# Optimization experiments

Measured on AMD Instinct MI355X. Metric: run time of the kernel, lower is better.

The kernel has to match this reference:

```python
import jax, jax.numpy as jnp
import numpy as np

B, S, E, H = 2, 4096, 512, 8
D = E // H  # head_dim = 64

def setup_inputs() -> dict:
    key = jax.random.key(0)
    k1, k2 = jax.random.split(key)
    x_local = jax.random.normal(k1, (B, S, E), dtype=jnp.float32)
    # torch nn.Linear weight layout: [out_features, in_features] = [3E, E]
    W_qkv = jax.random.normal(k2, (3 * E, E), dtype=jnp.float32) * (1.0 / np.sqrt(E))
    return {"x_local": x_local, "W_qkv": W_qkv, "segment_len": 2048, "dilation": 1}

def reference(x_local, W_qkv, segment_len, dilation):
    b, s, e = x_local.shape
    h, d = H, D
    # qkv projection (no bias), then split into per-head q,k,v: [b,h,s,d]
    qkv = jnp.einsum('bse,fe->bsf', x_local, W_qkv)
    qkv = qkv.reshape(b, s, 3, h, d).transpose(2, 0, 3, 1, 4)
    q, k, v = qkv[0], qkv[1], qkv[2]
    # dilation==1 -> no slicing branch; world_size==1 -> plain SDPA (no mask)
    scale = 1.0 / np.sqrt(d)
    scores = jnp.einsum('bhqd,bhkd->bhqk', q, k) * scale  # [b,h,s,s]
    attn = jax.nn.softmax(scores, axis=-1)
    out = jnp.einsum('bhqk,bhkd->bhqd', attn, v)
    # [b,h,s,d] -> [b,s,e]
    return out.transpose(0, 2, 1, 3).reshape(b, s, e)
```

## Files before the change

kernel.cpp:

```cpp
#include <hip/hip_runtime.h>
#include <stdint.h>

#define BB 2
#define SS 4096
#define EE 512
#define HH 8
#define DD 64
#define BH 16
#define M_ROWS 8192
#define N_COLS 1536
#define K_DIM 512

typedef unsigned short u16;
typedef unsigned int u32;
typedef __attribute__((ext_vector_type(8))) __bf16 bf16x8;
typedef __attribute__((ext_vector_type(4))) float f32x4;
typedef __attribute__((ext_vector_type(16))) float f32x16;

__device__ __forceinline__ u16 f2bf(float f) {
  u32 u = __float_as_uint(f);
  u32 r = u + 0x7fffu + ((u >> 16) & 1u);
  return (u16)(r >> 16);
}

__device__ __forceinline__ u32 cvtpk(float a, float b) {
  u32 r;
  asm("v_cvt_pk_bf16_f32 %0, %1, %2" : "=v"(r) : "v"(a), "v"(b));
  return r;
}

__device__ __forceinline__ float exp2f_fast(float x) {
  float r;
  asm("v_exp_f32 %0, %1" : "=v"(r) : "v"(x));
  return r;
}

__device__ __forceinline__ void gl_lds16(const void* g, void* l) {
  using gu32 = const __attribute__((address_space(1))) uint32_t;
  using lu32 = __attribute__((address_space(3))) uint32_t;
  __builtin_amdgcn_global_load_lds((gu32*)(uintptr_t)g,
                                   (lu32*)(uint32_t)(uintptr_t)l, 16, 0, 0);
}

__global__ __launch_bounds__(256) void cvt_f32_bf16(const float* __restrict__ src,
                                                    u16* __restrict__ dst, int n) {
  int stride = gridDim.x * blockDim.x * 4;
  for (int i = (blockIdx.x * blockDim.x + threadIdx.x) * 4; i < n; i += stride) {
    float4 v = *(const float4*)(src + i);
    u32 lo = (u32)f2bf(v.x) | ((u32)f2bf(v.y) << 16);
    u32 hi = (u32)f2bf(v.z) | ((u32)f2bf(v.w) << 16);
    uint2 p; p.x = lo; p.y = hi;
    *(uint2*)(dst + i) = p;
  }
}

#define BM 128
#define BN 128
#define BK 64

__global__ __launch_bounds__(256, 3) void qkv_gemm(const u16* __restrict__ Xb,
                                                   const u16* __restrict__ Wb,
                                                   u16* __restrict__ Qg,
                                                   u16* __restrict__ Kg,
                                                   u16* __restrict__ Vt) {
  __shared__ __align__(16) u16 SH[BM * BK * 2];
  u16* Al = SH;
  u16* Bl = SH + BM * BK;

  const int tid = threadIdx.x;
  const int lane = tid & 63;
  const int w = tid >> 6;
  const int wr = w >> 1, wc = w & 1;

  const int flat = blockIdx.x;
  const int sw = (flat & 7) * 96 + (flat >> 3);
  const int bx = sw & 63, by = sw >> 6;
  const int m0 = bx * BM;
  const int n0 = by * BN;

  f32x4 acc[4][4] = {};

  auto STAGE = [&](int kt) {
#pragma unroll
    for (int i = 0; i < 4; i++) {
      int chunk = w * 4 + i;
      int row = chunk * 8 + (lane >> 3);
      int seg = (lane & 7) ^ (row & 7);
      gl_lds16(Xb + (size_t)(m0 + row) * K_DIM + kt * BK + seg * 8, Al + chunk * 512);
      gl_lds16(Wb + (size_t)(n0 + row) * K_DIM + kt * BK + seg * 8, Bl + chunk * 512);
    }
  };

  const int NKT = K_DIM / BK;
  for (int kt = 0; kt < NKT; ++kt) {
    __syncthreads();
    STAGE(kt);
    asm volatile("s_waitcnt vmcnt(0)" ::: "memory");
    __syncthreads();

#pragma unroll
    for (int ks = 0; ks < 2; ++ks) {
      bf16x8 af[4], bfr[4];
#pragma unroll
      for (int t = 0; t < 4; t++) {
        int row = wr * 64 + t * 16 + (lane & 15);
        int byte = row * 128 + (((ks * 64) + (lane >> 4) * 16) ^ ((row & 7) << 4));
        af[t] = *(const bf16x8*)((const char*)Al + byte);
      }
#pragma unroll
      for (int t = 0; t < 4; t++) {
        int row = wc * 64 + t * 16 + (lane & 15);
        int byte = row * 128 + (((ks * 64) + (lane >> 4) * 16) ^ ((row & 7) << 4));
        bfr[t] = *(const bf16x8*)((const char*)Bl + byte);
      }
      __builtin_amdgcn_s_setprio(1);
#pragma unroll
      for (int am = 0; am < 4; am++)
#pragma unroll
        for (int bn = 0; bn < 4; bn++)
          acc[am][bn] = __builtin_amdgcn_mfma_f32_16x16x32_bf16(af[am], bfr[bn], acc[am][bn], 0, 0, 0);
      __builtin_amdgcn_s_setprio(0);
    }
  }

  const float qscale = 0.125f * 1.44269504f;
  if (by < 8) {
#pragma unroll
    for (int am = 0; am < 4; am++) {
      int mbase = m0 + wr * 64 + am * 16 + (lane >> 4) * 4;
#pragma unroll
      for (int bn = 0; bn < 4; bn++) {
        int n = n0 + wc * 64 + bn * 16 + (lane & 15);
        int which = n >> 9;
        int hh = (n >> 6) & 7, dd = n & 63;
        int b = mbase >> 12;
        int bh = b * HH + hh;
        u16* dst = (which == 0) ? Qg : Kg;
        float sc = (which == 0) ? qscale : 1.0f;
#pragma unroll
        for (int i = 0; i < 4; i++) {
          int s = (mbase + i) & 4095;
          dst[((size_t)bh * SS + s) * DD + dd] = f2bf(acc[am][bn][i] * sc);
        }
      }
    }
  } else {
    __syncthreads();
#pragma unroll
    for (int am = 0; am < 4; am++) {
      int mloc = wr * 64 + am * 16 + (lane >> 4) * 4;
#pragma unroll
      for (int bn = 0; bn < 4; bn++) {
        int nl = wc * 64 + bn * 16 + (lane & 15);
        union { u16 h[4]; uint2 u; } pk;
#pragma unroll
        for (int i = 0; i < 4; i++) pk.h[i] = f2bf(acc[am][bn][i]);
        int byte = nl * 256 + ((mloc * 2) ^ ((nl & 7) << 4));
        *(uint2*)((char*)SH + byte) = pk.u;
      }
    }
    __syncthreads();
    const int b = m0 >> 12;
#pragma unroll
    for (int i = 0; i < 8; i++) {
      int c = i * 256 + tid;
      int row = c >> 4, ch = c & 15;
      int byte = row * 256 + ((ch * 16) ^ ((row & 7) << 4));
      uint4 v = *(const uint4*)((const char*)SH + byte);
      int ng = n0 + row;
      int hh = (ng >> 6) & 7, dd = ng & 63;
      *(uint4*)(Vt + ((size_t)(b * HH + hh) * DD + dd) * SS + (m0 & 4095) + ch * 8) = v;
    }
  }
}

#define KVB 64
#define NT (SS / KVB)
#define SPLIT 2
#define HT (NT / SPLIT)

__global__ __launch_bounds__(256, 3) void flash_attn(const u16* __restrict__ Qg,
                                                     const u16* __restrict__ Kg,
                                                     const u16* __restrict__ Vt,
                                                     float* __restrict__ Opart,
                                                     float* __restrict__ Ml) {
  __shared__ __align__(16) char smem[32768];

  const int tid = threadIdx.x;
  const int lane = tid & 63;
  const int w = tid >> 6;
  const int hi = lane >> 5;
  const int lq = lane & 31;
  const int flat = blockIdx.x;
  const int sw = ((flat & 7) << 7) | (flat >> 3);
  const int qx = sw & 31;
  const int bhz = sw >> 5;
  const int bh = bhz >> 1;
  const int z = bhz & 1;
  const int q0 = qx * 128 + w * 32;

  bf16x8 qf[4];
  {
    const u16* qp = Qg + ((size_t)bh * SS + q0 + lq) * DD + hi * 8;
#pragma unroll
    for (int ks = 0; ks < 4; ks++) qf[ks] = *(const bf16x8*)(qp + ks * 16);
  }

  int loff[8];
#pragma unroll
  for (int ks = 0; ks < 4; ks++) {
    int col = ks * 32 + hi * 16;
    loff[ks * 2 + 0] = lq * 128 + (col ^ ((lq & 7) << 4));
    loff[ks * 2 + 1] = (32 + lq) * 128 + (col ^ ((lq & 7) << 4));
  }

  f32x16 oa0 = {}, oa1 = {};
  float m = -1e30f, l = 0.f;

  auto STAGE = [&](int kt, int buf) {
    char* kb = smem + buf * 16384;
    char* vb = kb + 8192;
#pragma unroll
    for (int i = 0; i < 2; i++) {
      int chunk = w * 2 + i;
      int row = chunk * 8 + (lane >> 3);
      int seg = (lane & 7) ^ (row & 7);
      gl_lds16(Kg + ((size_t)bh * SS + (size_t)kt * KVB + row) * DD + seg * 8,
               kb + chunk * 1024);
      gl_lds16(Vt + ((size_t)bh * DD + row) * SS + (size_t)kt * KVB + seg * 8,
               vb + chunk * 1024);
    }
  };

  STAGE(z * HT, 0);
  asm volatile("s_waitcnt vmcnt(0)" ::: "memory");
  __syncthreads();

  for (int t = 0; t < HT; ++t) {
    const int cur = t & 1;
    const char* Kc = smem + cur * 16384;
    const char* Vc = Kc + 8192;

    if (t + 1 < HT) STAGE(z * HT + t + 1, cur ^ 1);

    f32x16 sa0 = {}, sa1 = {};
    __builtin_amdgcn_s_setprio(1);
#pragma unroll
    for (int ks = 0; ks < 4; ks++) {
      bf16x8 kf0 = *(const bf16x8*)(Kc + loff[ks * 2 + 0]);
      bf16x8 kf1 = *(const bf16x8*)(Kc + loff[ks * 2 + 1]);
      sa0 = __builtin_amdgcn_mfma_f32_32x32x16_bf16(kf0, qf[ks], sa0, 0, 0, 0);
      sa1 = __builtin_amdgcn_mfma_f32_32x32x16_bf16(kf1, qf[ks], sa1, 0, 0, 0);
    }
    __builtin_amdgcn_s_setprio(0);

    float c0 = fmaxf(fmaxf(sa0[0], sa0[1]), sa0[2]);
    float c1 = fmaxf(fmaxf(sa0[8], sa0[9]), sa0[10]);
    float c2 = fmaxf(fmaxf(sa1[0], sa1[1]), sa1[2]);
    float c3 = fmaxf(fmaxf(sa1[8], sa1[9]), sa1[10]);
    c0 = fmaxf(fmaxf(c0, sa0[3]), sa0[4]);
    c1 = fmaxf(fmaxf(c1, sa0[11]), sa0[12]);
    c2 = fmaxf(fmaxf(c2, sa1[3]), sa1[4]);
    c3 = fmaxf(fmaxf(c3, sa1[11]), sa1[12]);
    c0 = fmaxf(fmaxf(c0, sa0[5]), sa0[6]);
    c1 = fmaxf(fmaxf(c1, sa0[13]), sa0[14]);
    c2 = fmaxf(fmaxf(c2, sa1[5]), sa1[6]);
    c3 = fmaxf(fmaxf(c3, sa1[13]), sa1[14]);
    c0 = fmaxf(fmaxf(c0, sa0[7]), c2);
    c1 = fmaxf(fmaxf(c1, sa0[15]), c3);
    c0 = fmaxf(fmaxf(c0, sa1[7]), sa1[15]);
    float tm = fmaxf(c0, c1);
    tm = fmaxf(tm, __shfl_xor(tm, 32));
    if (__any(tm > m + 8.f)) {
      float mnew = fmaxf(m, tm);
      float al = exp2f_fast(m - mnew);
      m = mnew;
      l *= al;
      oa0 *= al;
      oa1 *= al;
    }
    sa0 = sa0 - m;
    sa1 = sa1 - m;
#pragma unroll
    for (int r = 0; r < 16; r++) {
      sa0[r] = exp2f_fast(sa0[r]);
      sa1[r] = exp2f_fast(sa1[r]);
    }
    {
      f32x16 ps = sa0 + sa1;
      float rs = (((ps[0] + ps[1]) + (ps[2] + ps[3])) + ((ps[4] + ps[5]) + (ps[6] + ps[7])))
               + (((ps[8] + ps[9]) + (ps[10] + ps[11])) + ((ps[12] + ps[13]) + (ps[14] + ps[15])));
      l += rs;
    }

    bf16x8 paf[4];
#pragma unroll
    for (int kb = 0; kb < 2; kb++) {
#pragma unroll
      for (int h2 = 0; h2 < 2; h2++) {
        int base = h2 * 8;
        u32 a0, b0, a1, b1;
        if (kb == 0) {
          a0 = cvtpk(sa0[base + 0], sa0[base + 1]);
          b0 = cvtpk(sa0[base + 4], sa0[base + 5]);
          a1 = cvtpk(sa0[base + 2], sa0[base + 3]);
          b1 = cvtpk(sa0[base + 6], sa0[base + 7]);
        } else {
          a0 = cvtpk(sa1[base + 0], sa1[base + 1]);
          b0 = cvtpk(sa1[base + 4], sa1[base + 5]);
          a1 = cvtpk(sa1[base + 2], sa1[base + 3]);
          b1 = cvtpk(sa1[base + 6], sa1[base + 7]);
        }
        asm("v_permlane32_swap_b32 %0, %1" : "+v"(a0), "+v"(b0));
        asm("v_permlane32_swap_b32 %0, %1" : "+v"(a1), "+v"(b1));
        union { u32 d[4]; bf16x8 v; } u;
        u.d[0] = a0; u.d[1] = a1; u.d[2] = b0; u.d[3] = b1;
        paf[kb * 2 + h2] = u.v;
      }
    }

    __builtin_amdgcn_s_setprio(1);
#pragma unroll
    for (int ks = 0; ks < 4; ks++) {
      bf16x8 vf0 = *(const bf16x8*)(Vc + loff[ks * 2 + 0]);
      bf16x8 vf1 = *(const bf16x8*)(Vc + loff[ks * 2 + 1]);
      oa0 = __builtin_amdgcn_mfma_f32_32x32x16_bf16(vf0, paf[ks], oa0, 0, 0, 0);
      oa1 = __builtin_amdgcn_mfma_f32_32x32x16_bf16(vf1, paf[ks], oa1, 0, 0, 0);
    }
    __builtin_amdgcn_s_setprio(0);

    asm volatile("s_waitcnt vmcnt(0)" ::: "memory");
    __syncthreads();
  }

  l += __shfl_xor(l, 32);
  if (hi == 0)
    *(float2*)(Ml + ((size_t)(z * BH + bh) * SS + q0 + lq) * 2) = make_float2(m, l);

  float* ow = (float*)(smem + w * 8192);
#pragma unroll
  for (int db = 0; db < 2; db++)
#pragma unroll
    for (int r = 0; r < 16; r++) {
      int d = db * 32 + (r & 3) + 8 * (r >> 2) + 4 * hi;
      float v = db ? oa1[r] : oa0[r];
      *(float*)((char*)ow + lq * 256 + ((d * 4) ^ ((lq & 7) << 4))) = v;
    }
  __syncthreads();
#pragma unroll
  for (int i = 0; i < 8; i++) {
    int c = i * 64 + lane;
    int row = c >> 4, ch = c & 15;
    float4 v = *(const float4*)((const char*)ow + row * 256 + ((ch * 16) ^ ((row & 7) << 4)));
    *(float4*)(Opart + ((size_t)(z * BH + bh) * SS + q0 + row) * DD + ch * 4) = v;
  }
}

__global__ __launch_bounds__(256) void merge_split(const float* __restrict__ Opart,
                                                   const float* __restrict__ Ml,
                                                   float* __restrict__ Out) {
  int idx = blockIdx.x * 256 + threadIdx.x;
  int dq = idx & 15;
  int s = (idx >> 4) & (SS - 1);
  int bh = idx >> 16;
  float2 ml0 = *(const float2*)(Ml + ((size_t)bh * SS + s) * 2);
  float2 ml1 = *(const float2*)(Ml + ((size_t)(BH + bh) * SS + s) * 2);
  float M = fmaxf(ml0.x, ml1.x);
  float e0 = exp2f_fast(ml0.x - M);
  float e1 = exp2f_fast(ml1.x - M);
  float rden = 1.0f / (ml0.y * e0 + ml1.y * e1);
  e0 *= rden; e1 *= rden;
  float4 o0 = *(const float4*)(Opart + ((size_t)bh * SS + s) * DD + dq * 4);
  float4 o1 = *(const float4*)(Opart + ((size_t)(BH + bh) * SS + s) * DD + dq * 4);
  float4 o;
  o.x = o0.x * e0 + o1.x * e1;
  o.y = o0.y * e0 + o1.y * e1;
  o.z = o0.z * e0 + o1.z * e1;
  o.w = o0.w * e0 + o1.w * e1;
  int b = bh >> 3, hh = bh & 7;
  *(float4*)(Out + ((size_t)b * SS + s) * EE + hh * DD + dq * 4) = o;
}

extern "C" void kernel_launch(void* const* d_in, const int* in_sizes, int n_in,
                              void* d_out, int out_size, void* d_ws, size_t ws_size,
                              hipStream_t stream) {
  const float* x = (const float*)d_in[0];
  const float* Wq = (const float*)d_in[1];

  u16* xb = (u16*)d_ws;
  u16* wb = xb + (size_t)M_ROWS * K_DIM;
  u16* Qg = wb + (size_t)N_COLS * K_DIM;
  u16* Kg = Qg + (size_t)BH * SS * DD;
  u16* Vt = Kg + (size_t)BH * SS * DD;
  float* Opart = (float*)(Vt + (size_t)BH * SS * DD);
  float* Ml = Opart + (size_t)SPLIT * BH * SS * DD;

  cvt_f32_bf16<<<2048, 256, 0, stream>>>(x, xb, M_ROWS * K_DIM);
  cvt_f32_bf16<<<768, 256, 0, stream>>>(Wq, wb, N_COLS * K_DIM);

  qkv_gemm<<<768, 256, 0, stream>>>(xb, wb, Qg, Kg, Vt);

  flash_attn<<<1024, 256, 0, stream>>>(Qg, Kg, Vt, Opart, Ml);

  merge_split<<<4096, 256, 0, stream>>>(Opart, Ml, (float*)d_out);
}
```

Before: 190.2 us.

## Split KV into four chunks and store partial outputs in bf16

Raises the flash-attention KV split from two to four, doubling the grid to 2048 blocks, each handling half as many KV tiles. Partial outputs are now written as bf16 instead of fp32 to keep the intermediate traffic from growing. The merge kernel combines four partials with log-sum-exp rescaling. This trades more merge work and bf16 rounding of partials for more parallelism and shorter per-block work on the GPU.

```diff
diff --git a/kernel.cpp b/kernel.cpp
--- a/kernel.cpp
+++ b/kernel.cpp
@@ -35,6 +35,10 @@
   return r;
 }
 
+__device__ __forceinline__ float bf2f(u16 h) {
+  return __uint_as_float((u32)h << 16);
+}
+
 __device__ __forceinline__ void gl_lds16(const void* g, void* l) {
   using gu32 = const __attribute__((address_space(1))) uint32_t;
   using lu32 = __attribute__((address_space(3))) uint32_t;
@@ -176,13 +180,13 @@
 
 #define KVB 64
 #define NT (SS / KVB)
-#define SPLIT 2
+#define SPLIT 4
 #define HT (NT / SPLIT)
 
 __global__ __launch_bounds__(256, 3) void flash_attn(const u16* __restrict__ Qg,
                                                      const u16* __restrict__ Kg,
                                                      const u16* __restrict__ Vt,
-                                                     float* __restrict__ Opart,
+                                                     u16* __restrict__ Opart,
                                                      float* __restrict__ Ml) {
   __shared__ __align__(16) char smem[32768];
 
@@ -192,11 +196,11 @@
   const int hi = lane >> 5;
   const int lq = lane & 31;
   const int flat = blockIdx.x;
-  const int sw = ((flat & 7) << 7) | (flat >> 3);
+  const int sw = ((flat & 7) << 8) | (flat >> 3);
   const int qx = sw & 31;
   const int bhz = sw >> 5;
-  const int bh = bhz >> 1;
-  const int z = bhz & 1;
+  const int bh = bhz >> 2;
+  const int z = bhz & 3;
   const int q0 = qx * 128 + w * 32;
 
   bf16x8 qf[4];
@@ -352,31 +356,44 @@
     int c = i * 64 + lane;
     int row = c >> 4, ch = c & 15;
     float4 v = *(const float4*)((const char*)ow + row * 256 + ((ch * 16) ^ ((row & 7) << 4)));
-    *(float4*)(Opart + ((size_t)(z * BH + bh) * SS + q0 + row) * DD + ch * 4) = v;
-  }
-}
-
-__global__ __launch_bounds__(256) void merge_split(const float* __restrict__ Opart,
+    uint2 p; p.x = cvtpk(v.x, v.y); p.y = cvtpk(v.z, v.w);
+    *(uint2*)(Opart + ((size_t)(z * BH + bh) * SS + q0 + row) * DD + ch * 4) = p;
+  }
+}
+
+__global__ __launch_bounds__(256) void merge_split(const u16* __restrict__ Opart,
                                                    const float* __restrict__ Ml,
                                                    float* __restrict__ Out) {
   int idx = blockIdx.x * 256 + threadIdx.x;
   int dq = idx & 15;
   int s = (idx >> 4) & (SS - 1);
   int bh = idx >> 16;
-  float2 ml0 = *(const float2*)(Ml + ((size_t)bh * SS + s) * 2);
-  float2 ml1 = *(const float2*)(Ml + ((size_t)(BH + bh) * SS + s) * 2);
-  float M = fmaxf(ml0.x, ml1.x);
-  float e0 = exp2f_fast(ml0.x - M);
-  float e1 = exp2f_fast(ml1.x - M);
-  float rden = 1.0f / (ml0.y * e0 + ml1.y * e1);
-  e0 *= rden; e1 *= rden;
-  float4 o0 = *(const float4*)(Opart + ((size_t)bh * SS + s) * DD + dq * 4);
-  float4 o1 = *(const float4*)(Opart + ((size_t)(BH + bh) * SS + s) * DD + dq * 4);
-  float4 o;
-  o.x = o0.x * e0 + o1.x * e1;
-  o.y = o0.y * e0 + o1.y * e1;
-  o.z = o0.z * e0 + o1.z * e1;
-  o.w = o0.w * e0 + o1.w * e1;
+  float mv[SPLIT], lv[SPLIT];
+#pragma unroll
+  for (int i = 0; i < SPLIT; i++) {
+    float2 ml = *(const float2*)(Ml + ((size_t)(i * BH + bh) * SS + s) * 2);
+    mv[i] = ml.x; lv[i] = ml.y;
+  }
+  float M = fmaxf(fmaxf(mv[0], mv[1]), fmaxf(mv[2], mv[3]));
+  float den = 0.f;
+  float ei[SPLIT];
+#pragma unroll
+  for (int i = 0; i < SPLIT; i++) {
+    ei[i] = exp2f_fast(mv[i] - M);
+    den += lv[i] * ei[i];
+  }
+  float rden = 1.0f / den;
+  float4 o = make_float4(0.f, 0.f, 0.f, 0.f);
+#pragma unroll
+  for (int i = 0; i < SPLIT; i++) {
+    uint2 p = *(const uint2*)(Opart + ((size_t)(i * BH + bh) * SS + s) * DD + dq * 4);
+    float e = ei[i];
+    o.x += e * bf2f((u16)(p.x & 0xffff));
+    o.y += e * bf2f((u16)(p.x >> 16));
+    o.z += e * bf2f((u16)(p.y & 0xffff));
+    o.w += e * bf2f((u16)(p.y >> 16));
+  }
+  o.x *= rden; o.y *= rden; o.z *= rden; o.w *= rden;
   int b = bh >> 3, hh = bh & 7;
   *(float4*)(Out + ((size_t)b * SS + s) * EE + hh * DD + dq * 4) = o;
 }
@@ -392,15 +409,15 @@
   u16* Qg = wb + (size_t)N_COLS * K_DIM;
   u16* Kg = Qg + (size_t)BH * SS * DD;
   u16* Vt = Kg + (size_t)BH * SS * DD;
-  float* Opart = (float*)(Vt + (size_t)BH * SS * DD);
-  float* Ml = Opart + (size_t)SPLIT * BH * SS * DD;
+  u16* Opart = Vt + (size_t)BH * SS * DD;
+  float* Ml = (float*)(Opart + (size_t)SPLIT * BH * SS * DD);
 
   cvt_f32_bf16<<<2048, 256, 0, stream>>>(x, xb, M_ROWS * K_DIM);
   cvt_f32_bf16<<<768, 256, 0, stream>>>(Wq, wb, N_COLS * K_DIM);
 
   qkv_gemm<<<768, 256, 0, stream>>>(xb, wb, Qg, Kg, Vt);
 
-  flash_attn<<<1024, 256, 0, stream>>>(Qg, Kg, Vt, Opart, Ml);
+  flash_attn<<<2048, 256, 0, stream>>>(Qg, Kg, Vt, Opart, Ml);
 
   merge_split<<<4096, 256, 0, stream>>>(Opart, Ml, (float*)d_out);
 }
```

Result: no change. 192.1 us (+1.0%).
